# Kernel tuning notes

Measured on AMD Instinct MI355X. Metric: run time of the kernel, lower is better.

The kernel has to match this reference:

```python
import jax, jax.numpy as jnp
import numpy as np

TEMPERATURE = 0.01
STRIDE = 16  # original image coords -> feature grid (1024 / 64)


def setup_inputs() -> dict:
    key = jax.random.key(0)
    k1, k2, k3, k4, k5 = jax.random.split(key, 5)
    B, C, Hf, Wf, N = 32, 256, 64, 64, 64
    feats_src = jax.random.normal(k1, (B, C, Hf, Wf), dtype=jnp.float32)
    feats_trg = jax.random.normal(k2, (B, C, Hf, Wf), dtype=jnp.float32)
    # keypoints in original-image coordinates [0, 1024)
    kps_src = jax.random.uniform(k3, (B, N, 2), dtype=jnp.float32) * 1024.0
    kps_trg = jax.random.uniform(k4, (B, N, 2), dtype=jnp.float32) * 1024.0
    kps_mask = jax.random.bernoulli(k5, 0.7, (B, N))
    return {"feats_src": feats_src, "feats_trg": feats_trg,
            "kps_src": kps_src, "kps_trg": kps_trg, "kps_mask": kps_mask}


def _l2_normalize(x):
    # F.normalize(x, dim=1): x / max(||x||_2, eps)
    n = jnp.linalg.norm(x, axis=1, keepdims=True)
    return x / jnp.maximum(n, 1e-12)


def _kps_to_flat_idx(kps, Hf, Wf):
    # int(coord/16) truncation (coords >= 0 so trunc == floor), then clamp.
    fx = jnp.clip((kps[..., 0] / STRIDE).astype(jnp.int32), 0, Wf - 1)
    fy = jnp.clip((kps[..., 1] / STRIDE).astype(jnp.int32), 0, Hf - 1)
    return fy * Wf + fx  # (B, N)


def reference(feats_src, feats_trg, kps_src, kps_trg, kps_mask):
    B, C, Hf, Wf = feats_src.shape
    fs = _l2_normalize(feats_src).reshape(B, C, Hf * Wf)
    ft = _l2_normalize(feats_trg).reshape(B, C, Hf * Wf)

    src_idx = _kps_to_flat_idx(kps_src, Hf, Wf)  # (B, N)
    trg_idx = _kps_to_flat_idx(kps_trg, Hf, Wf)  # (B, N)

    # Gather query vectors at source keypoint cells: (B, C, N)
    queries = jnp.take_along_axis(fs, src_idx[:, None, :], axis=2)
    # Batched logits over all target cells: (B, N, Hf*Wf)
    logits = jnp.einsum('bcn,bcm->bnm', queries, ft) / TEMPERATURE

    logp = jax.nn.log_softmax(logits, axis=-1)
    nll = -jnp.take_along_axis(logp, trg_idx[..., None], axis=-1)[..., 0]  # (B, N)

    m = kps_mask.astype(nll.dtype)
    count = jnp.sum(m)
    # Masked mean over valid keypoints; 0 if no valid keypoints (matches torch).
    return jnp.sum(nll * m) / jnp.maximum(count, 1.0)
```

## Files before the change

### kernel.cpp

```cpp
#include <hip/hip_runtime.h>
#include <hip/hip_fp16.h>
#include <cstdint>

#define BB 32
#define CC 256
#define HF 64
#define WF 64
#define MM 4096
#define NN 64
#define MCHUNKS 16
#define MPB 256
#define KSTEPS 8
#define NBLK (BB * MCHUNKS)

typedef _Float16 half8 __attribute__((ext_vector_type(8)));
typedef __fp16 fp16x2 __attribute__((ext_vector_type(2)));
typedef float f32x4 __attribute__((ext_vector_type(4)));


__global__ void phase0_gather_norm(const float* __restrict__ fs,
                                   const float* __restrict__ kps_src,
                                   const float* __restrict__ kps_trg,
                                   const void* __restrict__ maskp,
                                   _Float16* __restrict__ wq,
                                   int* __restrict__ trgidx,
                                   float* __restrict__ minfoF,
                                   int* __restrict__ minfoI,
                                   float* __restrict__ out) {
  int blk = blockIdx.x;
  int b = blk >> 6, n = blk & 63;
  int c = threadIdx.x;

  float kx = kps_src[blk * 2 + 0];
  float ky = kps_src[blk * 2 + 1];
  int fx = min(max((int)(kx * (1.0f / 16.0f)), 0), WF - 1);
  int fy = min(max((int)(ky * (1.0f / 16.0f)), 0), HF - 1);
  int pix = fy * WF + fx;

  float x = fs[((size_t)b * CC + c) * MM + pix];

  float v = x * x;
  #pragma unroll
  for (int off = 32; off >= 1; off >>= 1) v += __shfl_xor(v, off);
  __shared__ float ssum[4];
  int wid = c >> 6, lane = c & 63;
  if (lane == 0) ssum[wid] = v;
  __syncthreads();
  float tot = ssum[0] + ssum[1] + ssum[2] + ssum[3];
  float inv = 1.0f / fmaxf(sqrtf(tot), 1e-12f);

  int ks = c >> 5, kg = (c >> 3) & 3, j = c & 7;
  int nt = n >> 4, nr = n & 15;
  int lane_f = kg * 16 + nr;
  size_t off = (size_t)b * 16384 + (size_t)((ks * 4 + nt) * 64 + lane_f) * 8 + j;
  wq[off] = (_Float16)(x * inv);

  if (c == 0) {
    float tx = kps_trg[blk * 2 + 0], ty = kps_trg[blk * 2 + 1];
    int gx = min(max((int)(tx * (1.0f / 16.0f)), 0), WF - 1);
    int gy = min(max((int)(ty * (1.0f / 16.0f)), 0), HF - 1);
    trgidx[blk] = gy * WF + gx;
  }

  if (blk == 0) {
    __shared__ int flagF, flagB;
    if (c == 0) { flagF = 0; flagB = 0; out[0] = 0.0f; }
    __syncthreads();
    const unsigned char* mb = (const unsigned char*)maskp;
    int lf = 0, lb = 0;
    for (int i = c; i < BB * NN; i += 256) {
      unsigned char vch = mb[i];
      int r = i & 3;
      if (r == 3 && vch == 0x3F) lf = 1;
      if (r != 0 && vch != 0) lb = 1;
    }
    if (lf) atomicOr(&flagF, 1);
    if (lb) atomicOr(&flagB, 1);
    __syncthreads();
    int layout = flagF ? 2 : (flagB ? 0 : 1);

    float lc = 0.f;
    for (int i = c; i < BB * NN; i += 256) {
      float mval;
      if (layout == 2) mval = ((const float*)maskp)[i];
      else if (layout == 0) mval = (float)mb[i];
      else mval = (float)((const int*)maskp)[i];
      lc += mval;
    }
    #pragma unroll
    for (int o2 = 32; o2 >= 1; o2 >>= 1) lc += __shfl_xor(lc, o2);
    __shared__ float cs[4];
    if (lane == 0) cs[wid] = lc;
    __syncthreads();
    if (c == 0) {
      minfoF[0] = cs[0] + cs[1] + cs[2] + cs[3];
      minfoI[1] = layout;
    }
  }
}

__global__ void __launch_bounds__(256)
phaseB(const float* __restrict__ ft,
       const _Float16* __restrict__ wq,
       const int* __restrict__ tidx,
       float* __restrict__ partM,
       float* __restrict__ partS,
       float* __restrict__ trgl) {
  __shared__ _Float16 qf[16384];
  __shared__ int trg_lds[NN];
  __shared__ float pM[4 * NN], pS[4 * NN];

  int b = blockIdx.x >> 4, mc = blockIdx.x & 15;
  int tid = threadIdx.x;

  const uint4* src = (const uint4*)(wq + (size_t)b * 16384);
  uint4* dst = (uint4*)qf;
  #pragma unroll
  for (int i = 0; i < 8; ++i) dst[tid + 256 * i] = src[tid + 256 * i];
  if (tid < NN) trg_lds[tid] = tidx[b * NN + tid];
  __syncthreads();

  int w = tid >> 6, lane = tid & 63, g = lane >> 4, col = lane & 15;
  int m0w = mc * MPB + w * 64;
  const float* fb = ft + (size_t)b * CC * MM;
  const float4* lb = (const float4*)(fb + (size_t)(g * 8) * MM + (m0w + 4 * col));
  #define ROW4 (MM / 4)

  f32x4 acc[4][4];
  #pragma unroll
  for (int jj = 0; jj < 4; ++jj)
    #pragma unroll
    for (int nt = 0; nt < 4; ++nt) acc[jj][nt] = (f32x4){0.f, 0.f, 0.f, 0.f};
  float ssq[4] = {0.f, 0.f, 0.f, 0.f};

  const half8* qv = (const half8*)qf;

  float4 cur[8], nxt[8];
  #pragma unroll
  for (int j = 0; j < 8; ++j) cur[j] = lb[(size_t)j * ROW4];

  #pragma unroll
  for (int ks = 0; ks < KSTEPS; ++ks) {
    if (ks + 1 < KSTEPS) {
      #pragma unroll
      for (int j = 0; j < 8; ++j)
        nxt[j] = lb[(size_t)((ks + 1) * 32 + j) * ROW4];
    }

    half8 qn0 = qv[(ks * 4 + 0) * 64 + lane];
    half8 qn1 = qv[(ks * 4 + 1) * 64 + lane];
    half8 qn2 = qv[(ks * 4 + 2) * 64 + lane];
    half8 qn3 = qv[(ks * 4 + 3) * 64 + lane];

    half8 aft[4];
    #pragma unroll
    for (int jj = 0; jj < 4; ++jj) {
      #pragma unroll
      for (int j = 0; j < 8; j += 2) {
        float u0 = cur[j][jj], u1 = cur[j + 1][jj];
        ssq[jj] += u0 * u0 + u1 * u1;
        fp16x2 h = __builtin_amdgcn_cvt_pkrtz(u0, u1);
        aft[jj][j] = (_Float16)h[0];
        aft[jj][j + 1] = (_Float16)h[1];
      }
    }

    #pragma unroll
    for (int jj = 0; jj < 4; ++jj) {
      acc[jj][0] = __builtin_amdgcn_mfma_f32_16x16x32_f16(aft[jj], qn0, acc[jj][0], 0, 0, 0);
      acc[jj][1] = __builtin_amdgcn_mfma_f32_16x16x32_f16(aft[jj], qn1, acc[jj][1], 0, 0, 0);
      acc[jj][2] = __builtin_amdgcn_mfma_f32_16x16x32_f16(aft[jj], qn2, acc[jj][2], 0, 0, 0);
      acc[jj][3] = __builtin_amdgcn_mfma_f32_16x16x32_f16(aft[jj], qn3, acc[jj][3], 0, 0, 0);
    }

    #pragma unroll
    for (int j = 0; j < 8; ++j) cur[j] = nxt[j];
  }

  #pragma unroll
  for (int jj = 0; jj < 4; ++jj) {
    ssq[jj] += __shfl_xor(ssq[jj], 16);
    ssq[jj] += __shfl_xor(ssq[jj], 32);
  }
  float sc[4][4];
  #pragma unroll
  for (int jj = 0; jj < 4; ++jj)
    #pragma unroll
    for (int r = 0; r < 4; ++r) {
      float t = __shfl(ssq[jj], 4 * g + r, 16);
      sc[jj][r] = 100.0f / fmaxf(sqrtf(t), 1e-12f);
    }

  #pragma unroll
  for (int nt = 0; nt < 4; ++nt) {
    int n = nt * 16 + col;
    int t = trg_lds[n];
    float v[4][4];
    #pragma unroll
    for (int jj = 0; jj < 4; ++jj)
      #pragma unroll
      for (int r = 0; r < 4; ++r)
        v[jj][r] = acc[jj][nt][r] * sc[jj][r];

    #pragma unroll
    for (int jj = 0; jj < 4; ++jj)
      #pragma unroll
      for (int r = 0; r < 4; ++r)
        if (t == m0w + 16 * g + 4 * r + jj) trgl[b * NN + n] = v[jj][r];

    float mx = -1e30f;
    #pragma unroll
    for (int jj = 0; jj < 4; ++jj)
      #pragma unroll
      for (int r = 0; r < 4; ++r) mx = fmaxf(mx, v[jj][r]);
    mx = fmaxf(mx, __shfl_xor(mx, 16));
    mx = fmaxf(mx, __shfl_xor(mx, 32));
    float s = 0.f;
    #pragma unroll
    for (int jj = 0; jj < 4; ++jj)
      #pragma unroll
      for (int r = 0; r < 4; ++r) s += __expf(v[jj][r] - mx);
    s += __shfl_xor(s, 16);
    s += __shfl_xor(s, 32);
    if (g == 0) { pM[w * NN + n] = mx; pS[w * NN + n] = s; }
  }
  __syncthreads();

  if (tid < NN) {
    int n = tid;
    float gm = fmaxf(fmaxf(pM[n], pM[NN + n]), fmaxf(pM[2 * NN + n], pM[3 * NN + n]));
    float S = 0.f;
    #pragma unroll
    for (int ww = 0; ww < 4; ++ww)
      S += pS[ww * NN + n] * __expf(pM[ww * NN + n] - gm);
    partM[(size_t)(b * NN + n) * MCHUNKS + mc] = gm;
    partS[(size_t)(b * NN + n) * MCHUNKS + mc] = S;
  }
}

__global__ void __launch_bounds__(256)
reduceFinal(const float* __restrict__ partM,
            const float* __restrict__ partS,
            const float* __restrict__ trgl,
            const void* __restrict__ maskp,
            const float* __restrict__ minfoF,
            const int* __restrict__ minfoI,
            float* __restrict__ out) {
  int tid = threadIdx.x;
  int p = blockIdx.x * 256 + tid;

  const float4* pm4 = (const float4*)(partM + (size_t)p * MCHUNKS);
  const float4* ps4 = (const float4*)(partS + (size_t)p * MCHUNKS);
  float gm = -1e30f, S = 0.f;
  #pragma unroll
  for (int q = 0; q < MCHUNKS / 4; ++q) {
    float4 m4 = pm4[q];
    float4 s4 = ps4[q];
    #pragma unroll
    for (int e = 0; e < 4; ++e) {
      float mi = ((const float*)&m4)[e];
      float si = ((const float*)&s4)[e];
      float nm = fmaxf(gm, mi);
      S = S * __expf(gm - nm) + si * __expf(mi - nm);
      gm = nm;
    }
  }
  float nll = gm + logf(S) - trgl[p];

  int layout = minfoI[1];
  const unsigned char* mb = (const unsigned char*)maskp;
  float mval;
  if (layout == 2) mval = ((const float*)maskp)[p];
  else if (layout == 0) mval = (float)mb[p];
  else mval = (float)((const int*)maskp)[p];

  float v = nll * mval;
  #pragma unroll
  for (int off = 32; off >= 1; off >>= 1) v += __shfl_xor(v, off);
  __shared__ float ps[4];
  int w = tid >> 6, lane = tid & 63;
  if (lane == 0) ps[w] = v;
  __syncthreads();
  if (tid == 0) {
    float s = ps[0] + ps[1] + ps[2] + ps[3];
    float cnt = minfoF[0];
    atomicAdd(out, s / fmaxf(cnt, 1.0f));
  }
}

extern "C" void kernel_launch(void* const* d_in, const int* in_sizes, int n_in,
                              void* d_out, int out_size, void* d_ws, size_t ws_size,
                              hipStream_t stream) {
  const float* fs   = (const float*)d_in[0];
  const float* ft   = (const float*)d_in[1];
  const float* ksrc = (const float*)d_in[2];
  const float* ktrg = (const float*)d_in[3];
  const void*  mask = d_in[4];
  float* out = (float*)d_out;

  _Float16* wq = (_Float16*)d_ws;
  float* partM = (float*)((char*)d_ws + (size_t)BB * 16384 * 2);
  float* partS = partM + (size_t)BB * NN * MCHUNKS;
  float* trgl  = partS + (size_t)BB * NN * MCHUNKS;
  int* tidx    = (int*)(trgl + BB * NN);
  float* minfoF = (float*)(tidx + BB * NN);
  int* minfoI   = (int*)minfoF;

  phase0_gather_norm<<<BB * NN, 256, 0, stream>>>(fs, ksrc, ktrg, mask, wq, tidx,
                                                  minfoF, minfoI, out);
  phaseB<<<NBLK, 256, 0, stream>>>(ft, wq, tidx, partM, partS, trgl);
  reduceFinal<<<BB * NN / 256, 256, 0, stream>>>(partM, partS, trgl, mask,
                                                 minfoF, minfoI, out);
}
```

Before: 54.07 us.

## Split phaseB work 2x2 across warps over M and N and double M chunks

Doubles the number of M chunks so each block covers 128 target cells instead of 256. The four warps are arranged as a 2x2 grid over M and N instead of all four splitting M. The register double-buffer prefetch is dropped, and `__launch_bounds__(256, 4)` is added to lower register use and raise occupancy and grid size for this memory-bound kernel. In exchange, warps sharing an M slice issue duplicate global loads of ft and repeat the fp16 conversion and sum-of-squares work. The per-batch query copy into LDS is also done by twice as many blocks.

```diff
diff --git a/kernel.cpp b/kernel.cpp
--- a/kernel.cpp
+++ b/kernel.cpp
@@ -8,8 +8,8 @@
 #define WF 64
 #define MM 4096
 #define NN 64
-#define MCHUNKS 16
-#define MPB 256
+#define MCHUNKS 32
+#define MPB 128
 #define KSTEPS 8
 #define NBLK (BB * MCHUNKS)
 
@@ -99,7 +99,7 @@
   }
 }
 
-__global__ void __launch_bounds__(256)
+__global__ void __launch_bounds__(256, 4)
 phaseB(const float* __restrict__ ft,
        const _Float16* __restrict__ wq,
        const int* __restrict__ tidx,
@@ -110,7 +110,7 @@
   __shared__ int trg_lds[NN];
   __shared__ float pM[4 * NN], pS[4 * NN];
 
-  int b = blockIdx.x >> 4, mc = blockIdx.x & 15;
+  int b = blockIdx.x >> 5, mc = blockIdx.x & 31;
   int tid = threadIdx.x;
 
   const uint4* src = (const uint4*)(wq + (size_t)b * 16384);
@@ -121,36 +121,26 @@
   __syncthreads();
 
   int w = tid >> 6, lane = tid & 63, g = lane >> 4, col = lane & 15;
-  int m0w = mc * MPB + w * 64;
+  int wm = w & 1, wn = w >> 1;
+  int m0w = mc * MPB + wm * 64;
   const float* fb = ft + (size_t)b * CC * MM;
   const float4* lb = (const float4*)(fb + (size_t)(g * 8) * MM + (m0w + 4 * col));
   #define ROW4 (MM / 4)
 
-  f32x4 acc[4][4];
+  f32x4 acc[4][2];
   #pragma unroll
   for (int jj = 0; jj < 4; ++jj)
     #pragma unroll
-    for (int nt = 0; nt < 4; ++nt) acc[jj][nt] = (f32x4){0.f, 0.f, 0.f, 0.f};
+    for (int ntl = 0; ntl < 2; ++ntl) acc[jj][ntl] = (f32x4){0.f, 0.f, 0.f, 0.f};
   float ssq[4] = {0.f, 0.f, 0.f, 0.f};
 
   const half8* qv = (const half8*)qf;
 
-  float4 cur[8], nxt[8];
-  #pragma unroll
-  for (int j = 0; j < 8; ++j) cur[j] = lb[(size_t)j * ROW4];
-
   #pragma unroll
   for (int ks = 0; ks < KSTEPS; ++ks) {
-    if (ks + 1 < KSTEPS) {
-      #pragma unroll
-      for (int j = 0; j < 8; ++j)
-        nxt[j] = lb[(size_t)((ks + 1) * 32 + j) * ROW4];
-    }
-
-    half8 qn0 = qv[(ks * 4 + 0) * 64 + lane];
-    half8 qn1 = qv[(ks * 4 + 1) * 64 + lane];
-    half8 qn2 = qv[(ks * 4 + 2) * 64 + lane];
-    half8 qn3 = qv[(ks * 4 + 3) * 64 + lane];
+    float4 cur[8];
+    #pragma unroll
+    for (int j = 0; j < 8; ++j) cur[j] = lb[(size_t)(ks * 32 + j) * ROW4];
 
     half8 aft[4];
     #pragma unroll
@@ -166,15 +156,12 @@
     }
 
     #pragma unroll
-    for (int jj = 0; jj < 4; ++jj) {
-      acc[jj][0] = __builtin_amdgcn_mfma_f32_16x16x32_f16(aft[jj], qn0, acc[jj][0], 0, 0, 0);
-      acc[jj][1] = __builtin_amdgcn_mfma_f32_16x16x32_f16(aft[jj], qn1, acc[jj][1], 0, 0, 0);
-      acc[jj][2] = __builtin_amdgcn_mfma_f32_16x16x32_f16(aft[jj], qn2, acc[jj][2], 0, 0, 0);
-      acc[jj][3] = __builtin_amdgcn_mfma_f32_16x16x32_f16(aft[jj], qn3, acc[jj][3], 0, 0, 0);
-    }
-
-    #pragma unroll
-    for (int j = 0; j < 8; ++j) cur[j] = nxt[j];
+    for (int ntl = 0; ntl < 2; ++ntl) {
+      half8 qn = qv[(ks * 4 + (wn * 2 + ntl)) * 64 + lane];
+      #pragma unroll
+      for (int jj = 0; jj < 4; ++jj)
+        acc[jj][ntl] = __builtin_amdgcn_mfma_f32_16x16x32_f16(aft[jj], qn, acc[jj][ntl], 0, 0, 0);
+    }
   }
 
   #pragma unroll
@@ -192,15 +179,16 @@
     }
 
   #pragma unroll
-  for (int nt = 0; nt < 4; ++nt) {
-    int n = nt * 16 + col;
+  for (int ntl = 0; ntl < 2; ++ntl) {
+    int nt2 = wn * 2 + ntl;
+    int n = nt2 * 16 + col;
     int t = trg_lds[n];
     float v[4][4];
     #pragma unroll
     for (int jj = 0; jj < 4; ++jj)
       #pragma unroll
       for (int r = 0; r < 4; ++r)
-        v[jj][r] = acc[jj][nt][r] * sc[jj][r];
+        v[jj][r] = acc[jj][ntl][r] * sc[jj][r];
 
     #pragma unroll
     for (int jj = 0; jj < 4; ++jj)
@@ -228,11 +216,11 @@
 
   if (tid < NN) {
     int n = tid;
-    float gm = fmaxf(fmaxf(pM[n], pM[NN + n]), fmaxf(pM[2 * NN + n], pM[3 * NN + n]));
-    float S = 0.f;
-    #pragma unroll
-    for (int ww = 0; ww < 4; ++ww)
-      S += pS[ww * NN + n] * __expf(pM[ww * NN + n] - gm);
+    int h = n >> 5;
+    float mA = pM[(2 * h + 0) * NN + n], mBv = pM[(2 * h + 1) * NN + n];
+    float sA = pS[(2 * h + 0) * NN + n], sBv = pS[(2 * h + 1) * NN + n];
+    float gm = fmaxf(mA, mBv);
+    float S = sA * __expf(mA - gm) + sBv * __expf(mBv - gm);
     partM[(size_t)(b * NN + n) * MCHUNKS + mc] = gm;
     partS[(size_t)(b * NN + n) * MCHUNKS + mc] = S;
   }
```

Measured after the change: 47.41 us. 1.14x faster.
